# Kernel tuning notes

Hardware: AMD Instinct MI355X
Metric: run time of the kernel (lower is better)

The kernel has to match this reference:

```python
import jax, jax.numpy as jnp
import numpy as np

N_EMBED = 384
N_HEAD = 6
HEAD_SIZE = N_EMBED // N_HEAD  # 64
LN_EPS = 1e-5


def setup_inputs() -> dict:
    key = jax.random.key(0)
    ks = jax.random.split(key, 12)
    B, T = 128, 256
    s_in = 1.0 / np.sqrt(N_EMBED)
    s_ff = 1.0 / np.sqrt(4 * N_EMBED)
    return {
        "x": jax.random.normal(ks[0], (B, T, N_EMBED), jnp.float32),
        "Wq": jax.random.normal(ks[1], (N_HEAD, N_EMBED, HEAD_SIZE), jnp.float32) * s_in,
        "Wk": jax.random.normal(ks[2], (N_HEAD, N_EMBED, HEAD_SIZE), jnp.float32) * s_in,
        "Wv": jax.random.normal(ks[3], (N_HEAD, N_EMBED, HEAD_SIZE), jnp.float32) * s_in,
        "Wproj": jax.random.normal(ks[4], (N_EMBED, N_EMBED), jnp.float32) * s_in,
        "bproj": jnp.zeros((N_EMBED,), jnp.float32),
        "W1": jax.random.normal(ks[5], (N_EMBED, 4 * N_EMBED), jnp.float32) * s_in,
        "b1": jnp.zeros((4 * N_EMBED,), jnp.float32),
        "W2": jax.random.normal(ks[6], (4 * N_EMBED, N_EMBED), jnp.float32) * s_ff,
        "b2": jnp.zeros((N_EMBED,), jnp.float32),
        "ln1_g": jnp.ones((N_EMBED,), jnp.float32),
        "ln1_b": jnp.zeros((N_EMBED,), jnp.float32),
        "ln2_g": jnp.ones((N_EMBED,), jnp.float32),
        "ln2_b": jnp.zeros((N_EMBED,), jnp.float32),
    }


def _layernorm(x, g, b):
    mu = jnp.mean(x, axis=-1, keepdims=True)
    var = jnp.mean(jnp.square(x - mu), axis=-1, keepdims=True)
    return (x - mu) * jax.lax.rsqrt(var + LN_EPS) * g + b


def _attention(xn, Wq, Wk, Wv, Wproj, bproj):
    B, T, C = xn.shape
    q = jnp.einsum("btc,hcd->bhtd", xn, Wq)
    k = jnp.einsum("btc,hcd->bhtd", xn, Wk)
    v = jnp.einsum("btc,hcd->bhtd", xn, Wv)
    # NOTE: original scales by C**-0.5 with C = n_embed (384), not head_size
    scores = jnp.einsum("bhtd,bhsd->bhts", q, k) * (C ** -0.5)
    causal = jnp.tril(jnp.ones((T, T), bool))
    scores = jnp.where(causal, scores, -jnp.inf)
    wei = jax.nn.softmax(scores, axis=-1)
    out = jnp.einsum("bhts,bhsd->bhtd", wei, v)
    out = out.transpose(0, 2, 1, 3).reshape(B, T, N_EMBED)  # concat heads
    return out @ Wproj + bproj


def reference(x, Wq, Wk, Wv, Wproj, bproj, W1, b1, W2, b2, ln1_g, ln1_b, ln2_g, ln2_b):
    x = x + _attention(_layernorm(x, ln1_g, ln1_b), Wq, Wk, Wv, Wproj, bproj)
    h = _layernorm(x, ln2_g, ln2_b)
    ff = jax.nn.relu(h @ W1 + b1) @ W2 + b2
    return x + ff
```

## Files before the change

kernel.cpp:

```cpp
#include <hip/hip_runtime.h>
#include <hip/hip_bf16.h>

typedef __hip_bfloat16 bf16;
typedef __attribute__((ext_vector_type(8))) short bf16x8;
typedef __attribute__((ext_vector_type(4))) float f32x4;

#define CEMB 384
#define NHEAD 6
#define HSZ 64
#define TSEQ 256
#define BATCH 128
#define MROWS (BATCH*TSEQ)
#define FDIM 1536
#define QSCALE 0.05103103630798288f
#define SMAX 8.0f

#define AS1 __attribute__((address_space(1)))
#define AS3 __attribute__((address_space(3)))
__device__ __forceinline__ void gload16(const void* g, void* l){
  __builtin_amdgcn_global_load_lds((const AS1 unsigned*)(g), (AS3 unsigned*)(l), 16, 0, 0);
}

__global__ __launch_bounds__(256) void ln_kernel(const float* __restrict__ x,
    const float* __restrict__ gam, const float* __restrict__ bet,
    bf16* __restrict__ y)
{
  const int row  = blockIdx.x*4 + (threadIdx.x>>6);
  const int lane = threadIdx.x & 63;
  const float* xr = x + (size_t)row*CEMB;
  float v[6]; float s = 0.f;
  #pragma unroll
  for (int i=0;i<6;i++){ v[i] = xr[lane + i*64]; s += v[i]; }
  #pragma unroll
  for (int m=1;m<64;m<<=1) s += __shfl_xor(s, m, 64);
  const float mu = s * (1.0f/CEMB);
  float qs = 0.f;
  #pragma unroll
  for (int i=0;i<6;i++){ v[i] -= mu; qs += v[i]*v[i]; }
  #pragma unroll
  for (int m=1;m<64;m<<=1) qs += __shfl_xor(qs, m, 64);
  const float rs = rsqrtf(qs*(1.0f/CEMB) + 1e-5f);
  bf16* yr = y + (size_t)row*CEMB;
  #pragma unroll
  for (int i=0;i<6;i++){
    int c = lane + i*64;
    yr[c] = __float2bfloat16(v[i]*rs*gam[c] + bet[c]);
  }
}

__global__ __launch_bounds__(256) void transpose_to_bf16(const float* __restrict__ src,
    bf16* __restrict__ dst, int K, int N)
{
  __shared__ float tile[32][33];
  const int n0 = blockIdx.x*32, k0 = blockIdx.y*32;
  src += (size_t)blockIdx.z*K*N;
  dst += (size_t)blockIdx.z*K*N;
  const int c = threadIdx.x & 31, r8 = threadIdx.x >> 5;
  #pragma unroll
  for (int i=0;i<4;i++)
    tile[r8 + i*8][c] = src[(size_t)(k0 + r8 + i*8)*N + n0 + c];
  __syncthreads();
  #pragma unroll
  for (int i=0;i<4;i++)
    dst[(size_t)(n0 + r8 + i*8)*K + k0 + c] = __float2bfloat16(tile[c][r8 + i*8]);
}

__global__ __launch_bounds__(256) void transpose_qkv(const float* __restrict__ Wq,
    const float* __restrict__ Wk, const float* __restrict__ Wv, bf16* __restrict__ dst)
{
  __shared__ float tile[32][33];
  const int z = blockIdx.z;
  const float* src = (z < 6) ? Wq : (z < 12 ? Wk : Wv);
  src += (size_t)(z % 6) * CEMB * HSZ;
  dst += (size_t)z * CEMB * HSZ;
  const int n0 = blockIdx.x*32, k0 = blockIdx.y*32;
  const int c = threadIdx.x & 31, r8 = threadIdx.x >> 5;
  #pragma unroll
  for (int i=0;i<4;i++)
    tile[r8 + i*8][c] = src[(size_t)(k0 + r8 + i*8)*HSZ + n0 + c];
  __syncthreads();
  #pragma unroll
  for (int i=0;i<4;i++)
    dst[(size_t)(n0 + r8 + i*8)*CEMB + k0 + c] = __float2bfloat16(tile[c][r8 + i*8]);
}

template<int EPI, int NN>
__global__ __launch_bounds__(256) void gemm_bt(
    const bf16* __restrict__ A, const bf16* __restrict__ BT, int K,
    const float* __restrict__ bias, const float* __restrict__ resid,
    float* __restrict__ outf, bf16* __restrict__ outb0,
    bf16* __restrict__ outb1, bf16* __restrict__ outb2)
{
  __shared__ char ldsA[2][128*128];
  __shared__ char ldsB[2][128*128];
  const int cpx = gridDim.x >> 3;
  const int wg  = (blockIdx.x & 7)*cpx + (blockIdx.x >> 3);
  const int bm = (wg / NN)*128, bn = (wg % NN)*128;
  const int t = threadIdx.x, lane = t & 63, wid = t >> 6;
  const int wr = (wid>>1)*64, wc = (wid&1)*64;
  const int g = lane >> 4, fr = lane & 15;
  const int N = NN*128;
  const int lrow = lane >> 3;
  const int scol = ((lane & 7) ^ lrow) << 4;
  f32x4 acc[4][4] = {};
  const int nk = K >> 6;
  const size_t rowK2 = (size_t)K*2;
  const char* Ab = (const char*)A + (size_t)(bm + wid*32 + lrow)*rowK2 + scol;
  const char* Bb = (const char*)BT + (size_t)(bn + wid*32 + lrow)*rowK2 + scol;

  auto stage = [&](int buf, int kt){
    const size_t ko = (size_t)kt*128;
    #pragma unroll
    for (int i=0;i<4;i++){
      gload16(Ab + (size_t)i*8*rowK2 + ko, ldsA[buf] + (wid*32 + i*8)*128);
      gload16(Bb + (size_t)i*8*rowK2 + ko, ldsB[buf] + (wid*32 + i*8)*128);
    }
  };

  stage(0, 0);
  stage(1, 1);
  asm volatile("s_waitcnt vmcnt(8)" ::: "memory");
  __builtin_amdgcn_s_barrier();
  for (int kt=0; kt<nk; ++kt){
    const int cur = kt & 1;
    #pragma unroll
    for (int ks=0; ks<2; ++ks){
      bf16x8 af[4], bfrag[4];
      #pragma unroll
      for (int mi=0;mi<4;mi++)
        af[mi] = *(const bf16x8*)(ldsA[cur] + (wr+mi*16+fr)*128 + (((ks*4+g)*16) ^ ((fr&7)<<4)));
      #pragma unroll
      for (int nj=0;nj<4;nj++)
        bfrag[nj] = *(const bf16x8*)(ldsB[cur] + (wc+nj*16+fr)*128 + (((ks*4+g)*16) ^ ((fr&7)<<4)));
      __builtin_amdgcn_s_setprio(1);
      #pragma unroll
      for (int mi=0;mi<4;mi++)
        #pragma unroll
        for (int nj=0;nj<4;nj++)
          acc[mi][nj] = __builtin_amdgcn_mfma_f32_16x16x32_bf16(af[mi], bfrag[nj], acc[mi][nj], 0, 0, 0);
      __builtin_amdgcn_s_setprio(0);
    }
    __builtin_amdgcn_s_barrier();
    if (kt+2 < nk) stage(cur, kt+2);
    if (kt+1 < nk){
      if (kt+2 < nk) asm volatile("s_waitcnt vmcnt(8)" ::: "memory");
      else           asm volatile("s_waitcnt vmcnt(0)" ::: "memory");
      __builtin_amdgcn_s_barrier();
    }
  }
  #pragma unroll
  for (int mi=0;mi<4;mi++)
    #pragma unroll
    for (int nj=0;nj<4;nj++)
      #pragma unroll
      for (int e=0;e<4;e++){
        const int m = bm + wr + mi*16 + 4*g + e;
        const int n = bn + wc + nj*16 + fr;
        const float vacc = acc[mi][nj][e];
        if constexpr (EPI==0){
          int sel = n/CEMB; int nn = n - sel*CEMB;
          int hh = nn>>6, dd = nn&63;
          int bb = m>>8,  tt = m&255;
          bf16 val = __float2bfloat16(sel==0 ? vacc * QSCALE : vacc);
          bf16* dst = sel==0 ? outb0 : (sel==1 ? outb1 : outb2);
          dst[((size_t)(bb*NHEAD + hh)*TSEQ + tt)*HSZ + dd] = val;
        } else if constexpr (EPI==1 || EPI==3){
          outf[(size_t)m*N + n] = vacc + bias[n] + resid[(size_t)m*N + n];
        } else {
          float z = vacc + bias[n];
          outb0[(size_t)m*N + n] = __float2bfloat16(z > 0.f ? z : 0.f);
        }
      }
}

__global__ __launch_bounds__(256) void attn_kernel(
    const bf16* __restrict__ q, const bf16* __restrict__ k,
    const bf16* __restrict__ v, bf16* __restrict__ out)
{
  __shared__ char kt_lds[64*128];
  __shared__ char vt_lds[80*128];
  __shared__ char p_lds[4][64*128];
  const int bh = blockIdx.x;
  const int bidx = bh / NHEAD, hidx = bh - bidx*NHEAD;
  const int t = threadIdx.x, lane = t & 63, w = t >> 6;
  const int g = lane >> 4, fr = lane & 15;
  const int lrow = lane >> 3;
  const int scol = ((lane & 7) ^ lrow) << 4;
  const size_t base = (size_t)bh * TSEQ * HSZ;

  if (t < 128){
    unsigned int ones2 = 0x3F803F80u;
    uint4 vv;
    if ((t>>3) == 0) vv = uint4{ones2, ones2, ones2, ones2};
    else             vv = uint4{0u, 0u, 0u, 0u};
    *(uint4*)(vt_lds + (64 + (t>>3))*128 + (t&7)*16) = vv;
  }

  bf16x8 qf[4][2];
  #pragma unroll
  for (int mi=0;mi<4;mi++)
    #pragma unroll
    for (int ks=0;ks<2;ks++)
      qf[mi][ks] = *(const bf16x8*)(q + base + (size_t)(w*64 + mi*16 + fr)*HSZ + ks*32 + g*8);

  f32x4 of[4][5] = {};

  for (int j=0;j<4;j++){
    __syncthreads();
    #pragma unroll
    for (int i=0;i<2;i++){
      int r0 = w*16 + i*8;
      gload16((const char*)(k + base + (size_t)(j*64 + r0 + lrow)*HSZ) + scol,
              kt_lds + r0*128);
    }
    #pragma unroll
    for (int i=0;i<2;i++){
      int chunk = t + i*256, r = chunk>>3, c = chunk&7;
      uint4 vv = *(const uint4*)(v + base + (size_t)(j*64 + r)*HSZ + c*8);
      const unsigned short* pv = (const unsigned short*)&vv;
      #pragma unroll
      for (int u=0;u<8;u++)
        *(unsigned short*)(vt_lds + (c*8+u)*128 + ((((r>>3) ^ u ^ c)&7)<<4) + (r&7)*2) = pv[u];
    }
    __syncthreads();
    if (j <= w){
      f32x4 sa[4][4] = {};
      #pragma unroll
      for (int ks=0;ks<2;ks++){
        bf16x8 kf[4];
        #pragma unroll
        for (int nj=0;nj<4;nj++)
          kf[nj] = *(const bf16x8*)(kt_lds + (nj*16+fr)*128 + (((ks*4+g)*16) ^ ((fr&7)<<4)));
        __builtin_amdgcn_s_setprio(1);
        #pragma unroll
        for (int mi=0;mi<4;mi++)
          #pragma unroll
          for (int nj=0;nj<4;nj++)
            sa[mi][nj] = __builtin_amdgcn_mfma_f32_16x16x32_bf16(qf[mi][ks], kf[nj], sa[mi][nj], 0, 0, 0);
        __builtin_amdgcn_s_setprio(0);
      }
      if (j == w){
        #pragma unroll
        for (int mi=0;mi<4;mi++)
          #pragma unroll
          for (int nj=0;nj<4;nj++)
            #pragma unroll
            for (int e=0;e<4;e++)
              if (nj*16 + fr > mi*16 + 4*g + e) sa[mi][nj][e] = -1e30f;
      }
      char* pl = p_lds[w];
      #pragma unroll
      for (int mi=0;mi<4;mi++)
        #pragma unroll
        for (int nj=0;nj<4;nj++)
          #pragma unroll
          for (int e=0;e<4;e++){
            int row = mi*16 + 4*g + e, col = nj*16 + fr;
            float p = __expf(sa[mi][nj][e] - SMAX);
            *(bf16*)(pl + row*128 + (((col>>3) ^ (row&7))<<4) + (col&7)*2) =
                __float2bfloat16(p);
          }
      #pragma unroll
      for (int ks=0;ks<2;ks++){
        bf16x8 pa[4], vf[5];
        #pragma unroll
        for (int mi=0;mi<4;mi++)
          pa[mi] = *(const bf16x8*)(pl + (mi*16+fr)*128 + (((ks*4+g)*16) ^ ((fr&7)<<4)));
        #pragma unroll
        for (int nd=0;nd<5;nd++){
          int d = nd*16 + fr;
          vf[nd] = *(const bf16x8*)(vt_lds + d*128 +
                   ((((ks*4+g) ^ (d&7) ^ ((d>>3)&7))&7)<<4));
        }
        __builtin_amdgcn_s_setprio(1);
        #pragma unroll
        for (int mi=0;mi<4;mi++)
          #pragma unroll
          for (int nd=0;nd<5;nd++)
            of[mi][nd] = __builtin_amdgcn_mfma_f32_16x16x32_bf16(pa[mi], vf[nd], of[mi][nd], 0, 0, 0);
        __builtin_amdgcn_s_setprio(0);
      }
    }
  }
  #pragma unroll
  for (int mi=0;mi<4;mi++){
    float rl[4];
    #pragma unroll
    for (int e=0;e<4;e++){
      float l = __shfl(of[mi][4][e], (int)(lane & 48), 64);
      rl[e] = 1.0f / l;
    }
    #pragma unroll
    for (int nd=0;nd<4;nd++)
      #pragma unroll
      for (int e=0;e<4;e++){
        int row = w*64 + mi*16 + 4*g + e;
        int d = nd*16 + fr;
        out[(size_t)(bidx*TSEQ + row)*CEMB + hidx*HSZ + d] =
            __float2bfloat16(of[mi][nd][e] * rl[e]);
      }
  }
}

extern "C" void kernel_launch(void* const* d_in, const int* in_sizes, int n_in,
                              void* d_out, int out_size, void* d_ws, size_t ws_size,
                              hipStream_t stream)
{
  const float* x     = (const float*)d_in[0];
  const float* Wq    = (const float*)d_in[1];
  const float* Wk    = (const float*)d_in[2];
  const float* Wv    = (const float*)d_in[3];
  const float* Wproj = (const float*)d_in[4];
  const float* bproj = (const float*)d_in[5];
  const float* W1    = (const float*)d_in[6];
  const float* b1    = (const float*)d_in[7];
  const float* W2    = (const float*)d_in[8];
  const float* b2    = (const float*)d_in[9];
  const float* ln1g  = (const float*)d_in[10];
  const float* ln1b  = (const float*)d_in[11];
  const float* ln2g  = (const float*)d_in[12];
  const float* ln2b  = (const float*)d_in[13];

  char* ws = (char*)d_ws;
  const size_t SA = (size_t)MROWS*CEMB*2;
  bf16* xn1    = (bf16*)(ws + 0*SA);
  bf16* qb     = (bf16*)(ws + 1*SA);
  bf16* kbuf   = (bf16*)(ws + 2*SA);
  bf16* vb     = (bf16*)(ws + 3*SA);
  bf16* attn_o = (bf16*)(ws + 0*SA);
  bf16* act    = (bf16*)(ws + 0*SA);
  bf16* hb     = (bf16*)(ws + 4*SA);
  float* x1    = (float*)(ws + 5*SA);
  char* wb     = ws + 5*SA + (size_t)MROWS*CEMB*4;
  bf16* qkvT   = (bf16*)wb;
  bf16* projT  = (bf16*)(wb + (size_t)1152*384*2);
  bf16* w1T    = (bf16*)(wb + (size_t)(1152+384)*384*2);
  bf16* w2T    = (bf16*)(wb + (size_t)(1152+384+1536)*384*2);

  dim3 blk(256);
  transpose_qkv<<<dim3(2,12,18), blk, 0, stream>>>(Wq, Wk, Wv, qkvT);
  transpose_to_bf16<<<dim3(12,12,1), blk, 0, stream>>>(Wproj, projT, CEMB, CEMB);
  transpose_to_bf16<<<dim3(48,12,1), blk, 0, stream>>>(W1,    w1T,   CEMB, FDIM);
  transpose_to_bf16<<<dim3(12,48,1), blk, 0, stream>>>(W2,    w2T,   FDIM, CEMB);

  ln_kernel<<<dim3(MROWS/4), blk, 0, stream>>>(x, ln1g, ln1b, xn1);
  gemm_bt<0,9><<<dim3(2304), blk, 0, stream>>>(xn1, qkvT, CEMB, nullptr, nullptr,
                                               nullptr, qb, kbuf, vb);
  attn_kernel<<<dim3(768), blk, 0, stream>>>(qb, kbuf, vb, attn_o);
  gemm_bt<1,3><<<dim3(768), blk, 0, stream>>>(attn_o, projT, CEMB, bproj, x,
                                              x1, nullptr, nullptr, nullptr);
  ln_kernel<<<dim3(MROWS/4), blk, 0, stream>>>(x1, ln2g, ln2b, hb);
  gemm_bt<2,12><<<dim3(3072), blk, 0, stream>>>(hb, w1T, CEMB, b1, nullptr,
                                                nullptr, act, nullptr, nullptr);
  gemm_bt<3,3><<<dim3(768), blk, 0, stream>>>(act, w2T, FDIM, b2, x1,
                                              (float*)d_out, nullptr, nullptr, nullptr);
}
```

Measured before the change: 283.8 us.

## Keep full-K A row-block resident in LDS and sweep N tiles per workgroup

For the K=384 GEMMs (QKV, proj, FF1), each workgroup now loads its entire 128x384 A block into LDS once and loops over all N tiles, streaming B tiles through a 3-deep buffer. The grid shrinks to 256 workgroups, one per M block, so A is fetched from global memory only once. The FF2 GEMM becomes a dedicated kernel with a 4-stage B/A pipeline and one fewer barrier per k-step. The cost is heavy LDS use (about 144KB per workgroup), which allows only one workgroup per CU, and a fixed grid of 256 workgroups.

```diff
diff --git a/kernel.cpp b/kernel.cpp
--- a/kernel.cpp
+++ b/kernel.cpp
@@ -85,26 +85,120 @@
 }
 
 template<int EPI, int NN>
-__global__ __launch_bounds__(256) void gemm_bt(
-    const bf16* __restrict__ A, const bf16* __restrict__ BT, int K,
+__global__ __launch_bounds__(256) void ares_gemm(
+    const bf16* __restrict__ A, const bf16* __restrict__ BT,
     const float* __restrict__ bias, const float* __restrict__ resid,
     float* __restrict__ outf, bf16* __restrict__ outb0,
     bf16* __restrict__ outb1, bf16* __restrict__ outb2)
 {
-  __shared__ char ldsA[2][128*128];
-  __shared__ char ldsB[2][128*128];
+  constexpr int T = NN*6;
+  constexpr int N = NN*128;
+  __shared__ char lA[128*768];
+  __shared__ char lB[3][128*128];
+  const int bm = blockIdx.x*128;
+  const int t = threadIdx.x, lane = t & 63, w = t >> 6;
+  const int wr = (w>>1)*64, wc = (w&1)*64;
+  const int g = lane >> 4, fr = lane & 15, x7 = fr & 7;
+
+  #pragma unroll
+  for (int i=0;i<24;i++){
+    int s0 = i*256 + w*64;
+    int sl = s0 + lane;
+    int row = sl/48, b = sl - row*48;
+    gload16((const char*)A + (size_t)(bm+row)*768 + ((b ^ (row&7))<<4), lA + s0*16);
+  }
+  auto stageB = [&](int s2){
+    int bn2 = s2/6, kt2 = s2 - bn2*6, bf = s2 % 3;
+    #pragma unroll
+    for (int i=0;i<4;i++){
+      int s0 = i*256 + w*64;
+      int sl = s0 + lane;
+      int row = sl>>3, b = sl&7;
+      gload16((const char*)BT + (size_t)(bn2*128+row)*768 + kt2*128 + ((b ^ (row&7))<<4),
+              lB[bf] + s0*16);
+    }
+  };
+  stageB(0); stageB(1);
+  asm volatile("s_waitcnt vmcnt(4)" ::: "memory");
+  __builtin_amdgcn_s_barrier();
+
+  int rA[4], rB[4];
+  #pragma unroll
+  for (int i=0;i<4;i++){ rA[i] = (wr+i*16+fr)*768; rB[i] = (wc+i*16+fr)*128; }
+  const int CC0 = ((0*4+g) ^ x7) << 4;
+  const int CC1 = ((1*4+g) ^ x7) << 4;
+
+  #pragma unroll 1
+  for (int bn=0; bn<NN; ++bn){
+    f32x4 acc[4][4] = {};
+    #pragma unroll 1
+    for (int kt=0; kt<6; ++kt){
+      const int s = bn*6 + kt, buf = s % 3;
+      const int ktoff = kt*128;
+      #pragma unroll
+      for (int ks2=0; ks2<2; ++ks2){
+        const int cc = ks2 ? CC1 : CC0;
+        bf16x8 af[4], bq[4];
+        #pragma unroll
+        for (int mi=0;mi<4;mi++) af[mi] = *(const bf16x8*)(lA + rA[mi] + ktoff + cc);
+        #pragma unroll
+        for (int nj=0;nj<4;nj++) bq[nj] = *(const bf16x8*)(lB[buf] + rB[nj] + cc);
+        __builtin_amdgcn_s_setprio(1);
+        #pragma unroll
+        for (int mi=0;mi<4;mi++)
+          #pragma unroll
+          for (int nj=0;nj<4;nj++)
+            acc[mi][nj] = __builtin_amdgcn_mfma_f32_16x16x32_bf16(af[mi], bq[nj], acc[mi][nj], 0, 0, 0);
+        __builtin_amdgcn_s_setprio(0);
+      }
+      if (s+2 < T){ stageB(s+2); asm volatile("s_waitcnt vmcnt(4)" ::: "memory"); }
+      else if (s+1 < T){ asm volatile("s_waitcnt vmcnt(0)" ::: "memory"); }
+      __builtin_amdgcn_s_barrier();
+    }
+    #pragma unroll
+    for (int mi=0;mi<4;mi++)
+      #pragma unroll
+      for (int nj=0;nj<4;nj++)
+        #pragma unroll
+        for (int e=0;e<4;e++){
+          const int m = bm + wr + mi*16 + 4*g + e;
+          const int n = bn*128 + wc + nj*16 + fr;
+          const float vacc = acc[mi][nj][e];
+          if constexpr (EPI==0){
+            int sel = n/CEMB; int nn = n - sel*CEMB;
+            int hh = nn>>6, dd = nn&63;
+            int bb = m>>8,  tt = m&255;
+            bf16 val = __float2bfloat16(sel==0 ? vacc * QSCALE : vacc);
+            bf16* dst = sel==0 ? outb0 : (sel==1 ? outb1 : outb2);
+            dst[((size_t)(bb*NHEAD + hh)*TSEQ + tt)*HSZ + dd] = val;
+          } else if constexpr (EPI==1){
+            outf[(size_t)m*N + n] = vacc + bias[n] + resid[(size_t)m*N + n];
+          } else {
+            float z = vacc + bias[n];
+            outb0[(size_t)m*N + n] = __float2bfloat16(z > 0.f ? z : 0.f);
+          }
+        }
+  }
+}
+
+__global__ __launch_bounds__(256) void gemm_ff2(
+    const bf16* __restrict__ A, const bf16* __restrict__ BT,
+    const float* __restrict__ bias, const float* __restrict__ resid,
+    float* __restrict__ outf)
+{
+  constexpr int NN = 3, nk = 24;
+  __shared__ char ldsA[4][128*128];
+  __shared__ char ldsB[4][128*128];
   const int cpx = gridDim.x >> 3;
   const int wg  = (blockIdx.x & 7)*cpx + (blockIdx.x >> 3);
   const int bm = (wg / NN)*128, bn = (wg % NN)*128;
   const int t = threadIdx.x, lane = t & 63, wid = t >> 6;
   const int wr = (wid>>1)*64, wc = (wid&1)*64;
   const int g = lane >> 4, fr = lane & 15;
-  const int N = NN*128;
   const int lrow = lane >> 3;
   const int scol = ((lane & 7) ^ lrow) << 4;
   f32x4 acc[4][4] = {};
-  const int nk = K >> 6;
-  const size_t rowK2 = (size_t)K*2;
+  const size_t rowK2 = (size_t)FDIM*2;
   const char* Ab = (const char*)A + (size_t)(bm + wid*32 + lrow)*rowK2 + scol;
   const char* Bb = (const char*)BT + (size_t)(bn + wid*32 + lrow)*rowK2 + scol;
 
@@ -117,12 +211,11 @@
     }
   };
 
-  stage(0, 0);
-  stage(1, 1);
-  asm volatile("s_waitcnt vmcnt(8)" ::: "memory");
+  stage(0,0); stage(1,1); stage(2,2);
+  asm volatile("s_waitcnt vmcnt(16)" ::: "memory");
   __builtin_amdgcn_s_barrier();
   for (int kt=0; kt<nk; ++kt){
-    const int cur = kt & 1;
+    const int cur = kt & 3;
     #pragma unroll
     for (int ks=0; ks<2; ++ks){
       bf16x8 af[4], bfrag[4];
@@ -140,13 +233,15 @@
           acc[mi][nj] = __builtin_amdgcn_mfma_f32_16x16x32_bf16(af[mi], bfrag[nj], acc[mi][nj], 0, 0, 0);
       __builtin_amdgcn_s_setprio(0);
     }
+    if (kt+3 < nk){
+      stage((kt+3)&3, kt+3);
+      asm volatile("s_waitcnt vmcnt(16)" ::: "memory");
+    } else if (kt+2 < nk){
+      asm volatile("s_waitcnt vmcnt(8)" ::: "memory");
+    } else if (kt+1 < nk){
+      asm volatile("s_waitcnt vmcnt(0)" ::: "memory");
+    }
     __builtin_amdgcn_s_barrier();
-    if (kt+2 < nk) stage(cur, kt+2);
-    if (kt+1 < nk){
-      if (kt+2 < nk) asm volatile("s_waitcnt vmcnt(8)" ::: "memory");
-      else           asm volatile("s_waitcnt vmcnt(0)" ::: "memory");
-      __builtin_amdgcn_s_barrier();
-    }
   }
   #pragma unroll
   for (int mi=0;mi<4;mi++)
@@ -156,20 +251,7 @@
       for (int e=0;e<4;e++){
         const int m = bm + wr + mi*16 + 4*g + e;
         const int n = bn + wc + nj*16 + fr;
-        const float vacc = acc[mi][nj][e];
-        if constexpr (EPI==0){
-          int sel = n/CEMB; int nn = n - sel*CEMB;
-          int hh = nn>>6, dd = nn&63;
-          int bb = m>>8,  tt = m&255;
-          bf16 val = __float2bfloat16(sel==0 ? vacc * QSCALE : vacc);
-          bf16* dst = sel==0 ? outb0 : (sel==1 ? outb1 : outb2);
-          dst[((size_t)(bb*NHEAD + hh)*TSEQ + tt)*HSZ + dd] = val;
-        } else if constexpr (EPI==1 || EPI==3){
-          outf[(size_t)m*N + n] = vacc + bias[n] + resid[(size_t)m*N + n];
-        } else {
-          float z = vacc + bias[n];
-          outb0[(size_t)m*N + n] = __float2bfloat16(z > 0.f ? z : 0.f);
-        }
+        outf[(size_t)m*CEMB + n] = acc[mi][nj][e] + bias[n] + resid[(size_t)m*CEMB + n];
       }
 }
 
@@ -344,14 +426,13 @@
   transpose_to_bf16<<<dim3(12,48,1), blk, 0, stream>>>(W2,    w2T,   FDIM, CEMB);
 
   ln_kernel<<<dim3(MROWS/4), blk, 0, stream>>>(x, ln1g, ln1b, xn1);
-  gemm_bt<0,9><<<dim3(2304), blk, 0, stream>>>(xn1, qkvT, CEMB, nullptr, nullptr,
-                                               nullptr, qb, kbuf, vb);
+  ares_gemm<0,9><<<dim3(256), blk, 0, stream>>>(xn1, qkvT, nullptr, nullptr,
+                                                nullptr, qb, kbuf, vb);
   attn_kernel<<<dim3(768), blk, 0, stream>>>(qb, kbuf, vb, attn_o);
-  gemm_bt<1,3><<<dim3(768), blk, 0, stream>>>(attn_o, projT, CEMB, bproj, x,
-                                              x1, nullptr, nullptr, nullptr);
+  ares_gemm<1,3><<<dim3(256), blk, 0, stream>>>(attn_o, projT, bproj, x,
+                                                x1, nullptr, nullptr, nullptr);
   ln_kernel<<<dim3(MROWS/4), blk, 0, stream>>>(x1, ln2g, ln2b, hb);
-  gemm_bt<2,12><<<dim3(3072), blk, 0, stream>>>(hb, w1T, CEMB, b1, nullptr,
-                                                nullptr, act, nullptr, nullptr);
-  gemm_bt<3,3><<<dim3(768), blk, 0, stream>>>(act, w2T, FDIM, b2, x1,
-                                              (float*)d_out, nullptr, nullptr, nullptr);
-}
+  ares_gemm<2,12><<<dim3(256), blk, 0, stream>>>(hb, w1T, b1, nullptr,
+                                                 nullptr, act, nullptr, nullptr);
+  gemm_ff2<<<dim3(768), blk, 0, stream>>>(act, w2T, b2, x1, (float*)d_out);
+}
```

After: 348.3 us. 22.7% more time.
